# Kernel tuning notes

Hardware: AMD Instinct MI355X
Metric: run time of the kernel (lower is better)

Reference implementation:

```python
import jax, jax.numpy as jnp
import numpy as np

B, S, D = 4, 1024, 1024
NH, DH = 16, 64
DI = 4096
EPS = 1e-5


def layer_norm(x, g, b):
    mu = jnp.mean(x, axis=-1, keepdims=True)
    var = jnp.mean(jnp.square(x - mu), axis=-1, keepdims=True)
    return (x - mu) * jax.lax.rsqrt(var + EPS) * g + b


def rel_shift(x):
    # x: [B, n, q, r] -> Transformer-XL relative shift + lower-tri mask
    b, n, q, r = x.shape
    zp = jnp.zeros((b, n, q, 1), x.dtype)
    xp = jnp.concatenate([zp, x], axis=3).reshape(b, n, r + 1, q)
    x = xp[:, :, 1:, :].reshape(b, n, q, r)
    tril = jnp.tril(jnp.ones((q, r), x.dtype), r - q)
    return x * tril[None, None]


def setup_inputs() -> dict:
    key = jax.random.key(0)
    ks = jax.random.split(key, 16)
    sc = 0.02
    return {
        "w": jax.random.normal(ks[0], (B, S, D), jnp.float32),
        "r": jax.random.normal(ks[1], (B, S, D), jnp.float32),
        "w_bias": jax.random.normal(ks[2], (NH, 1, DH), jnp.float32) * sc,
        "r_bias": jax.random.normal(ks[3], (NH, 1, DH), jnp.float32) * sc,
        "Wq": jax.random.normal(ks[4], (D, NH * DH), jnp.float32) * sc,
        "Wk": jax.random.normal(ks[5], (D, NH * DH), jnp.float32) * sc,
        "Wv": jax.random.normal(ks[6], (D, NH * DH), jnp.float32) * sc,
        "Wr": jax.random.normal(ks[7], (D, NH * DH), jnp.float32) * sc,
        "Wo": jax.random.normal(ks[8], (NH * DH, D), jnp.float32) * sc,
        "ln1_g": jnp.ones((D,), jnp.float32),
        "ln1_b": jnp.zeros((D,), jnp.float32),
        "W1": jax.random.normal(ks[9], (D, DI), jnp.float32) * sc,
        "b1": jnp.zeros((DI,), jnp.float32),
        "W2": jax.random.normal(ks[10], (DI, D), jnp.float32) * sc,
        "b2": jnp.zeros((D,), jnp.float32),
        "ln2_g": jnp.ones((D,), jnp.float32),
        "ln2_b": jnp.zeros((D,), jnp.float32),
    }


def reference(w, r, w_bias, r_bias, Wq, Wk, Wv, Wr, Wo,
              ln1_g, ln1_b, W1, b1, W2, b2, ln2_g, ln2_b):
    b, q_len, _ = w.shape
    k_len = q_len
    scale = 1.0 / (DH ** 0.5)

    def heads(x):
        return x.reshape(b, -1, NH, DH).transpose(0, 2, 1, 3)  # [B, n, S, d]

    q = heads(w @ Wq)
    k = heads(w @ Wk)
    v = heads(w @ Wv)
    rr = heads(r @ Wr)

    ac = jnp.einsum('bnid,bnjd->bnij', q + w_bias[None], k)
    bd = rel_shift(jnp.einsum('bnid,bnjd->bnij', q + r_bias[None], rr))
    attn_score = (ac + bd) * scale

    mask = jnp.triu(jnp.ones((q_len, k_len), bool), 1)
    attn_score = jnp.where(mask[None, None], jnp.float32(-1e9), attn_score)
    attn_prob = jax.nn.softmax(attn_score, axis=-1)

    attn_vec = jnp.einsum('bnij,bnjd->bnid', attn_prob, v)
    attn_vec = attn_vec.transpose(0, 2, 1, 3).reshape(b, q_len, NH * DH)
    attn_out = attn_vec @ Wo

    x = layer_norm(w + attn_out, ln1_g, ln1_b)
    ff = jax.nn.relu(x @ W1 + b1) @ W2 + b2
    return layer_norm(x + ff, ln2_g, ln2_b)
```

## Files before the change

### kernel.cpp

```cpp
#include <hip/hip_runtime.h>
#include <hip/hip_bf16.h>

using bf16 = __hip_bfloat16;
typedef __attribute__((ext_vector_type(8))) short bf16x8;
typedef __attribute__((ext_vector_type(4))) float f32x4;

static constexpr int TB  = 4;
static constexpr int TS  = 1024;
static constexpr int TD  = 1024;
static constexpr int TNH = 16;
static constexpr int TDH = 64;
static constexpr int TDI = 4096;

__device__ __forceinline__ void gll16(const bf16* g, bf16* l)
{
    __builtin_amdgcn_global_load_lds(
        (const __attribute__((address_space(1))) void*)g,
        (__attribute__((address_space(3))) void*)l, 16, 0, 0);
}

__global__ __launch_bounds__(256) void zero_out_k(float* __restrict__ out, long n)
{
    long i = (long)blockIdx.x * 256 + threadIdx.x;
    if (i < n) out[i] = 0.0f;
}

__global__ __launch_bounds__(256) void convert2_f2b(const float* __restrict__ a,
                                                    const float* __restrict__ b,
                                                    bf16* __restrict__ oa,
                                                    bf16* __restrict__ ob, long n)
{
    const float* src = blockIdx.y ? b : a;
    bf16* dst = blockIdx.y ? ob : oa;
    long i = ((long)blockIdx.x * 256 + threadIdx.x) * 8;
    if (i >= n) return;
    float4 f0 = *(const float4*)(src + i);
    float4 f1 = *(const float4*)(src + i + 4);
    bf16 t[8] = {__float2bfloat16(f0.x), __float2bfloat16(f0.y),
                 __float2bfloat16(f0.z), __float2bfloat16(f0.w),
                 __float2bfloat16(f1.x), __float2bfloat16(f1.y),
                 __float2bfloat16(f1.z), __float2bfloat16(f1.w)};
    *(bf16x8*)(dst + i) = *(bf16x8*)t;
}

__global__ __launch_bounds__(256) void transpose_f2b(const float* __restrict__ in,
                                                     bf16* __restrict__ out,
                                                     int R, int C)
{
    __shared__ float tile[32][33];
    int c0 = blockIdx.x * 32, r0 = blockIdx.y * 32;
    int tx = threadIdx.x & 31, ty = threadIdx.x >> 5;
#pragma unroll
    for (int dy = 0; dy < 32; dy += 8)
        tile[ty + dy][tx] = in[(long)(r0 + ty + dy) * C + (c0 + tx)];
    __syncthreads();
#pragma unroll
    for (int dy = 0; dy < 32; dy += 8)
        out[(long)(c0 + ty + dy) * R + (r0 + tx)] = __float2bfloat16(tile[tx][ty + dy]);
}

__global__ __launch_bounds__(256) void transpose5_f2b(const float* __restrict__ p0,
                                                      const float* __restrict__ p1,
                                                      const float* __restrict__ p2,
                                                      const float* __restrict__ p3,
                                                      const float* __restrict__ p4,
                                                      bf16* __restrict__ dstBase)
{
    __shared__ float tile[32][33];
    const int D = TD;
    int z = blockIdx.z;
    const float* in = (z == 0) ? p0 : (z == 1) ? p1 : (z == 2) ? p2 : (z == 3) ? p3 : p4;
    bf16* out = dstBase + (long)z * D * D;
    int c0 = blockIdx.x * 32, r0 = blockIdx.y * 32;
    int tx = threadIdx.x & 31, ty = threadIdx.x >> 5;
#pragma unroll
    for (int dy = 0; dy < 32; dy += 8)
        tile[ty + dy][tx] = in[(long)(r0 + ty + dy) * D + (c0 + tx)];
    __syncthreads();
#pragma unroll
    for (int dy = 0; dy < 32; dy += 8)
        out[(long)(c0 + ty + dy) * D + (r0 + tx)] = __float2bfloat16(tile[tx][ty + dy]);
}


__device__ __forceinline__ void stage_half(const bf16* __restrict__ X, long ldx,
                                           long rbase, long kcol,
                                           bf16* lds, int srow)
{
    gll16(X + (rbase + srow) * ldx + kcol, lds);
    gll16(X + (rbase + 128 + srow) * ldx + kcol, lds + 4096);
}

template<int MODE>
__global__ __launch_bounds__(512, 2) void gemm256_k(
    const bf16* __restrict__ A, long lda,
    const bf16* __restrict__ Bt, long ldb,
    bf16* __restrict__ O0, bf16* __restrict__ O1,
    bf16* __restrict__ O2, bf16* __restrict__ O3,
    const float* __restrict__ bias,
    int K, int GY, long ldc)
{
    __shared__ bf16 LDSbf[65536];

    const int NT = K >> 6;
    const int NI = NT >> 1;

    const int nwg = gridDim.x;
    const int orig = blockIdx.x;
    const int q = nwg >> 3, r = nwg & 7;
    const int xcd = orig & 7, idx = orig >> 3;
    const int wgid = (xcd < r ? xcd * (q + 1) : r * (q + 1) + (xcd - r) * q) + idx;

    int tx, ty;
    if (MODE == 1) {
        if (wgid < 192) { ty = wgid & 15; tx = wgid >> 4; }
        else { int w2 = wgid - 192; ty = 16 + (w2 & 15); tx = 12 + (w2 >> 4); }
    } else {
        ty = wgid % GY; tx = wgid / GY;
    }
    const long row0 = (long)ty * 256;
    const int col0 = tx * 256;

    const int tid = threadIdx.x;
    const int lane = tid & 63;
    const int wave = tid >> 6;
    const int wm2 = wave >> 2;
    const int wn4 = wave & 3;
    const int l15 = lane & 15;
    const int lq  = lane >> 4;

    const int slot = ((l15 & 1) << 2) | (lq ^ ((l15 >> 1) & 3));
    const int rdA = (wm2 * 64 + (l15 >> 1)) * 64 + slot * 8;
    const int rdB = 16384 + (wn4 * 32 + (l15 >> 1)) * 64 + slot * 8;

    const int srow  = wave * 16 + ((lane >> 3) << 1) + ((lane >> 2) & 1);
    const int scol8 = ((lane & 3) ^ ((lane >> 3) & 3)) * 8;

    f32x4 acc[8][4] = {};
    bf16x8 af[8], bb[4];

#define SA(t, db, kh) stage_half(A, lda, row0, (long)(t) * 64 + (kh) * 32 + scol8, \
                                 LDSbf + (db) * 32768 + (kh) * 8192 + wave * 512, srow)
#define SB(t, db, kh) stage_half(Bt, ldb, (long)col0, (long)(t) * 64 + (kh) * 32 + scol8, \
                                 LDSbf + (db) * 32768 + 16384 + (kh) * 8192 + wave * 512, srow)
#define RD_A(bp, kh) do {                                                              \
    _Pragma("unroll")                                                                  \
    for (int i_ = 0; i_ < 8; ++i_)                                                     \
        af[i_] = *(const bf16x8*)(LDSbf + (bp) * 32768 + (kh) * 8192 + rdA + i_ * 512);\
    } while (0)
#define RD_B(bp, kh, jh) do {                                                          \
    bb[(jh)*2]   = *(const bf16x8*)(LDSbf + (bp)*32768 + (kh)*8192 + rdB + ((jh)*2)*512);   \
    bb[(jh)*2+1] = *(const bf16x8*)(LDSbf + (bp)*32768 + (kh)*8192 + rdB + ((jh)*2+1)*512); \
    } while (0)
#define MM(jh) do {                                                                    \
    __builtin_amdgcn_s_setprio(1);                                                     \
    _Pragma("unroll")                                                                  \
    for (int i_ = 0; i_ < 8; ++i_) {                                                   \
        acc[i_][(jh)*2]   = __builtin_amdgcn_mfma_f32_16x16x32_bf16(af[i_], bb[(jh)*2],   acc[i_][(jh)*2],   0, 0, 0); \
        acc[i_][(jh)*2+1] = __builtin_amdgcn_mfma_f32_16x16x32_bf16(af[i_], bb[(jh)*2+1], acc[i_][(jh)*2+1], 0, 0, 0); \
    }                                                                                  \
    __builtin_amdgcn_s_setprio(0);                                                     \
    } while (0)
#define BAR       __builtin_amdgcn_s_barrier()
#define WLGKM0    do { asm volatile("s_waitcnt lgkmcnt(0)" ::: "memory");              \
                       __builtin_amdgcn_sched_barrier(0); } while (0)
#define WVM6      asm volatile("s_waitcnt vmcnt(6)" ::: "memory")

    SA(0, 0, 0); SB(0, 0, 0); SA(0, 0, 1); SB(0, 0, 1); SA(1, 1, 0);
    WVM6; BAR;

    for (int it = 0; it < NI; ++it) {
        const int T  = 2 * it;
        const int t1 = T + 1;
        const int t2 = (T + 2 < NT) ? T + 2 : NT - 1;
        const int t3 = (T + 3 < NT) ? T + 3 : NT - 1;

        RD_A(0, 0); RD_B(0, 0, 0); SB(t1, 1, 0);
        BAR; WLGKM0; MM(0); BAR;
        RD_B(0, 0, 1); SA(t1, 1, 1);
        BAR; WLGKM0; MM(1); WVM6; BAR;
        RD_A(0, 1); RD_B(0, 1, 0); SB(t1, 1, 1);
        BAR; WLGKM0; MM(0); BAR;
        RD_B(0, 1, 1); SA(t2, 0, 0);
        BAR; WLGKM0; MM(1); WVM6; BAR;
        RD_A(1, 0); RD_B(1, 0, 0); SB(t2, 0, 0);
        BAR; WLGKM0; MM(0); BAR;
        RD_B(1, 0, 1); SA(t2, 0, 1);
        BAR; WLGKM0; MM(1); WVM6; BAR;
        RD_A(1, 1); RD_B(1, 1, 0); SB(t2, 0, 1);
        BAR; WLGKM0; MM(0); BAR;
        RD_B(1, 1, 1); SA(t3, 1, 0);
        BAR; WLGKM0; MM(1); WVM6; BAR;
    }
    asm volatile("s_waitcnt vmcnt(0)" ::: "memory");

#undef SA
#undef SB
#undef RD_A
#undef RD_B
#undef MM
#undef BAR
#undef WLGKM0
#undef WVM6

    if (MODE == 1) {
        const int sel = tx >> 2;
        bf16* O = (sel == 0) ? O0 : (sel == 1) ? O1 : (sel == 2) ? O2 : O3;
        const int coladj = sel << 10;
        const long rowadj = (sel == 3) ? 4096 : 0;
#pragma unroll
        for (int i = 0; i < 8; ++i) {
            long mrow0 = row0 - rowadj + wm2 * 128 + i * 16 + lq * 4;
#pragma unroll
            for (int j = 0; j < 4; ++j) {
                int nc = col0 - coladj + wn4 * 64 + j * 16 + l15;
#pragma unroll
                for (int rg = 0; rg < 4; ++rg) {
                    float v = acc[i][j][rg];
                    if (sel == 0) v += bias[nc];
                    long mrow = mrow0 + rg;
                    long b_ = mrow >> 10;
                    int s  = (int)mrow & 1023;
                    int n_ = nc >> 6, d = nc & 63;
                    long pidx;
                    if (sel == 2) {
                        pidx = ((b_ * 16 + n_) << 16)
                             + ((d >> 4) * 128 + (s >> 3)) * 128 + (d & 15) * 8 + (s & 7);
                    } else {
                        pidx = ((b_ * 16 + n_) << 16)
                             + ((s >> 4) * 8 + (d >> 3)) * 128 + (s & 15) * 8 + (d & 7);
                    }
                    O[pidx] = __float2bfloat16(v);
                }
            }
        }
    } else {
#pragma unroll
        for (int i = 0; i < 8; ++i) {
            long rb = (row0 + wm2 * 128 + i * 16 + lq * 4) * ldc;
#pragma unroll
            for (int j = 0; j < 4; ++j) {
                int nc = col0 + wn4 * 64 + j * 16 + l15;
#pragma unroll
                for (int rg = 0; rg < 4; ++rg) {
                    float v = acc[i][j][rg] + bias[nc];
                    v = fmaxf(v, 0.0f);
                    O0[rb + (long)rg * ldc + nc] = __float2bfloat16(v);
                }
            }
        }
    }
}

template<int MODE>
__global__ __launch_bounds__(512, 2) void gemm128_k(
    const bf16* __restrict__ A, long lda,
    const bf16* __restrict__ Bt, long ldb,
    float* __restrict__ Zf,
    const float* __restrict__ residf, const bf16* __restrict__ residb,
    const float* __restrict__ bias,
    int K, int GY, long ldc)
{
    __shared__ bf16 LDSbf[32768];

    const int NT = K >> 6;
    const int NI = NT >> 1;

    const int nwg = gridDim.x;
    const int orig = blockIdx.x;
    const int q = nwg >> 3, r = nwg & 7;
    const int xcd = orig & 7, idx = orig >> 3;
    const int wgid = (xcd < r ? xcd * (q + 1) : r * (q + 1) + (xcd - r) * q) + idx;

    const int ty = wgid % GY, tx = wgid / GY;
    const long row0 = (long)ty * 128;
    const long col0 = (long)tx * 128;

    const int tid = threadIdx.x;
    const int lane = tid & 63;
    const int wave = tid >> 6;
    const int wm2 = wave >> 2;
    const int wn4 = wave & 3;
    const int l15 = lane & 15;
    const int lq  = lane >> 4;

    const int slot = ((l15 & 1) << 2) | (lq ^ ((l15 >> 1) & 3));
    const int rdA = (wm2 * 32 + (l15 >> 1)) * 64 + slot * 8;
    const int rdB = 8192 + (wn4 * 16 + (l15 >> 1)) * 64 + slot * 8;

    const int srow  = (tid >> 3) * 2 + ((tid >> 2) & 1);
    const int scol8 = ((tid & 3) ^ ((tid >> 3) & 3)) * 8;

    f32x4 acc[4][2] = {};
    bf16x8 af[4], bb[2];

#define SA(t, db, kh) gll16(A + (row0 + srow) * lda + (long)(t) * 64 + (kh) * 32 + scol8, \
                            LDSbf + (db) * 16384 + (kh) * 4096 + wave * 512)
#define SB(t, db, kh) gll16(Bt + (col0 + srow) * ldb + (long)(t) * 64 + (kh) * 32 + scol8, \
                            LDSbf + (db) * 16384 + 8192 + (kh) * 4096 + wave * 512)
#define RD(db, kh) do {                                                                \
    _Pragma("unroll")                                                                  \
    for (int i_ = 0; i_ < 4; ++i_)                                                     \
        af[i_] = *(const bf16x8*)(LDSbf + (db) * 16384 + (kh) * 4096 + rdA + i_ * 512);\
    _Pragma("unroll")                                                                  \
    for (int j_ = 0; j_ < 2; ++j_)                                                     \
        bb[j_] = *(const bf16x8*)(LDSbf + (db) * 16384 + (kh) * 4096 + rdB + j_ * 512);\
    } while (0)
#define MM8 do {                                                                       \
    __builtin_amdgcn_s_setprio(1);                                                     \
    _Pragma("unroll")                                                                  \
    for (int i_ = 0; i_ < 4; ++i_) {                                                   \
        acc[i_][0] = __builtin_amdgcn_mfma_f32_16x16x32_bf16(af[i_], bb[0], acc[i_][0], 0, 0, 0); \
        acc[i_][1] = __builtin_amdgcn_mfma_f32_16x16x32_bf16(af[i_], bb[1], acc[i_][1], 0, 0, 0); \
    }                                                                                  \
    __builtin_amdgcn_s_setprio(0);                                                     \
    } while (0)
#define BAR       __builtin_amdgcn_s_barrier()
#define WLGKM0    do { asm volatile("s_waitcnt lgkmcnt(0)" ::: "memory");              \
                       __builtin_amdgcn_sched_barrier(0); } while (0)
#define WVM4      asm volatile("s_waitcnt vmcnt(4)" ::: "memory")

    SA(0, 0, 0); SB(0, 0, 0); SA(0, 0, 1); SB(0, 0, 1); SA(1, 1, 0); SB(1, 1, 0);
    WVM4; BAR;

    for (int it = 0; it < NI; ++it) {
        const int T  = 2 * it;
        const int t1 = T + 1;
        const int t2 = (T + 2 < NT) ? T + 2 : NT - 1;
        const int t3 = (T + 3 < NT) ? T + 3 : NT - 1;

        RD(0, 0); SA(t1, 1, 1); SB(t1, 1, 1);
        BAR; WLGKM0; MM8; WVM4; BAR;
        RD(0, 1); SA(t2, 0, 0); SB(t2, 0, 0);
        BAR; WLGKM0; MM8; WVM4; BAR;
        RD(1, 0); SA(t2, 0, 1); SB(t2, 0, 1);
        BAR; WLGKM0; MM8; WVM4; BAR;
        RD(1, 1); SA(t3, 1, 0); SB(t3, 1, 0);
        BAR; WLGKM0; MM8; WVM4; BAR;
    }
    asm volatile("s_waitcnt vmcnt(0)" ::: "memory");

#undef SA
#undef SB
#undef RD
#undef MM8
#undef BAR
#undef WLGKM0
#undef WVM4

#pragma unroll
    for (int i = 0; i < 4; ++i) {
        long mrow0 = row0 + wm2 * 64 + i * 16 + lq * 4;
#pragma unroll
        for (int j = 0; j < 2; ++j) {
            int nc = (int)col0 + wn4 * 32 + j * 16 + l15;
#pragma unroll
            for (int rg = 0; rg < 4; ++rg) {
                long ridx = (mrow0 + rg) * ldc + nc;
                float v = acc[i][j][rg];
                if (MODE == 3) v += residf[ridx];
                else           v += bias[nc] + __bfloat162float(residb[ridx]);
                Zf[ridx] = v;
            }
        }
    }
}

__global__ __launch_bounds__(64, 4) void flash_attn(
    const bf16* __restrict__ Qpk, const bf16* __restrict__ Kpk,
    const bf16* __restrict__ RRpk, const bf16* __restrict__ Vpk,
    const float* __restrict__ wbias, const float* __restrict__ rbias,
    bf16* __restrict__ Oa)
{
    const int S = TS, D = TD;
    __shared__ bf16 scr[16 * 161];

    const int orig = blockIdx.x;
    const int xcd = orig & 7, idx = orig >> 3;
    const int bn = xcd * 8 + (idx & 7);
    const int rem = idx >> 3;
    const int r16 = 63 - rem;
    const int it = r16 >> 3;
    const int rowstart = r16 * 16;
    const int dwq = (r16 & 7) * 16;
    const int b = bn >> 4, n = bn & 15;

    const int lane = threadIdx.x;
    const int l15 = lane & 15, lq = lane >> 4;

    const bf16* Qb = Qpk  + (long)bn * 65536;
    const bf16* Kb = Kpk  + (long)bn * 65536;
    const bf16* Rb = RRpk + (long)bn * 65536;
    const bf16* Vb = Vpk  + (long)bn * 65536;

    bf16x8 afw[2], afr[2];
#pragma unroll
    for (int ks = 0; ks < 2; ++ks) {
        afw[ks] = *(const bf16x8*)(Qb + (r16 * 8 + ks * 4 + lq) * 128 + l15 * 8);
        bf16 tmp[8];
#pragma unroll
        for (int jj = 0; jj < 8; ++jj) {
            int di_ = n * 64 + ks * 32 + lq * 8 + jj;
            float f = __bfloat162float(((const bf16*)&afw[ks])[jj])
                      + rbias[di_] - wbias[di_];
            tmp[jj] = __float2bfloat16(f);
        }
        afr[ks] = *(bf16x8*)tmp;
    }

    float mst[4], lst[4];
    f32x4 Oacc[4] = {};
#pragma unroll
    for (int rg = 0; rg < 4; ++rg) { mst[rg] = -1e30f; lst[rg] = 0.0f; }

    const int cofs16 = 1008 - rowstart;

    for (int jt = 0; jt <= it; ++jt) {
        const int j0 = jt * 128;
        const int rbt = (j0 + cofs16) >> 4;

#pragma unroll
        for (int g = 0; g < 2; ++g) {
            const int NF = g ? 4 : 5;
            f32x4 bdl[5] = {};
#pragma unroll
            for (int ks = 0; ks < 2; ++ks) {
                bf16x8 bfr[5];
#pragma unroll
                for (int f = 0; f < 5; ++f) {
                    if (f < NF) {
                        int t = rbt + g * 5 + f;
                        if (t > 63) t = 63;
                        bfr[f] = *(const bf16x8*)(Rb + (t * 8 + ks * 4 + lq) * 128 + l15 * 8);
                    }
                }
#pragma unroll
                for (int f = 0; f < 5; ++f)
                    if (f < NF)
                        bdl[f] = __builtin_amdgcn_mfma_f32_16x16x32_bf16(
                            afr[ks], bfr[f], bdl[f], 0, 0, 0);
            }
#pragma unroll
            for (int f = 0; f < 5; ++f)
                if (f < NF)
#pragma unroll
                    for (int rg = 0; rg < 4; ++rg) {
                        int ldi = lq * 4 + rg;
                        scr[ldi * 161 + (g * 5 + f) * 16 + l15] =
                            __float2bfloat16(bdl[f][rg]);
                    }
        }

        f32x4 ac[8] = {};
#pragma unroll
        for (int ks = 0; ks < 2; ++ks) {
            bf16x8 bk[8];
#pragma unroll
            for (int f = 0; f < 8; ++f)
                bk[f] = *(const bf16x8*)(
                    Kb + (((j0 >> 4) + f) * 8 + ks * 4 + lq) * 128 + l15 * 8);
#pragma unroll
            for (int f = 0; f < 8; ++f)
                ac[f] = __builtin_amdgcn_mfma_f32_16x16x32_bf16(
                    afw[ks], bk[f], ac[f], 0, 0, 0);
        }

        const bool diag = (jt == it);
#pragma unroll
        for (int nf = 0; nf < 8; ++nf)
#pragma unroll
            for (int rg = 0; rg < 4; ++rg) {
                int ldi = lq * 4 + rg;
                int col = nf * 16 + l15;
                float bdv = __bfloat162float(scr[ldi * 161 + (col + 15 - ldi)]);
                float s = (ac[nf][rg] + bdv) * 0.125f;
                if (diag && (col > dwq + ldi)) s = -1e30f;
                ac[nf][rg] = s;
            }

        float alpha[4];
#pragma unroll
        for (int rg = 0; rg < 4; ++rg) {
            float v = -1e30f;
#pragma unroll
            for (int nf = 0; nf < 8; ++nf) v = fmaxf(v, ac[nf][rg]);
            for (int o = 8; o; o >>= 1) v = fmaxf(v, __shfl_xor(v, o));
            float mn = fmaxf(mst[rg], v);
            alpha[rg] = __expf(mst[rg] - mn);
            mst[rg] = mn;
        }
#pragma unroll
        for (int nf = 0; nf < 8; ++nf)
#pragma unroll
            for (int rg = 0; rg < 4; ++rg)
                ac[nf][rg] = __expf(ac[nf][rg] - mst[rg]);
#pragma unroll
        for (int rg = 0; rg < 4; ++rg) {
            float sv = 0.0f;
#pragma unroll
            for (int nf = 0; nf < 8; ++nf) sv += ac[nf][rg];
            for (int o = 8; o; o >>= 1) sv += __shfl_xor(sv, o);
            lst[rg] = lst[rg] * alpha[rg] + sv;
        }
#pragma unroll
        for (int nf = 0; nf < 4; ++nf)
#pragma unroll
            for (int rg = 0; rg < 4; ++rg)
                Oacc[nf][rg] *= alpha[rg];

#pragma unroll
        for (int nf = 0; nf < 8; ++nf)
#pragma unroll
            for (int rg = 0; rg < 4; ++rg) {
                int ldi = lq * 4 + rg;
                scr[ldi * 136 + nf * 16 + l15] = __float2bfloat16(ac[nf][rg]);
            }
#pragma unroll
        for (int ks2 = 0; ks2 < 4; ++ks2) {
            bf16x8 pa = *(const bf16x8*)(&scr[l15 * 136 + ks2 * 32 + lq * 8]);
            bf16x8 vb[4];
#pragma unroll
            for (int nf = 0; nf < 4; ++nf)
                vb[nf] = *(const bf16x8*)(
                    Vb + (nf * 128 + (j0 >> 3) + ks2 * 4 + lq) * 128 + l15 * 8);
#pragma unroll
            for (int nf = 0; nf < 4; ++nf)
                Oacc[nf] = __builtin_amdgcn_mfma_f32_16x16x32_bf16(
                    pa, vb[nf], Oacc[nf], 0, 0, 0);
        }
    }

#pragma unroll
    for (int rg = 0; rg < 4; ++rg) {
        float inv = 1.0f / lst[rg];
#pragma unroll
        for (int nf = 0; nf < 4; ++nf) {
            int row = rowstart + lq * 4 + rg;
            int col = nf * 16 + l15;
            Oa[((long)(b * S + row)) * D + n * 64 + col] =
                __float2bfloat16(Oacc[nf][rg] * inv);
        }
    }
}

__global__ __launch_bounds__(256) void ln_single(const float* __restrict__ Zf,
                                                 const float* __restrict__ g,
                                                 const float* __restrict__ beta,
                                                 float* __restrict__ Yf,
                                                 bf16* __restrict__ Yb)
{
    const int D = TD;
    long row = blockIdx.x;
    int tid = threadIdx.x;
    int wave = tid >> 6;

    float v[4], s = 0.0f;
#pragma unroll
    for (int it = 0; it < 4; ++it) {
        int c = tid + it * 256;
        float x = Zf[row * D + c];
        v[it] = x; s += x;
    }
    for (int off = 32; off; off >>= 1) s += __shfl_xor(s, off);
    __shared__ float sm[8];
    if ((tid & 63) == 0) sm[wave] = s;
    __syncthreads();
    float mean = (sm[0] + sm[1] + sm[2] + sm[3]) * (1.0f / D);

    float var = 0.0f;
#pragma unroll
    for (int it = 0; it < 4; ++it) { float d = v[it] - mean; var += d * d; }
    for (int off = 32; off; off >>= 1) var += __shfl_xor(var, off);
    if ((tid & 63) == 0) sm[4 + wave] = var;
    __syncthreads();
    var = (sm[4] + sm[5] + sm[6] + sm[7]) * (1.0f / D);
    float rinv = rsqrtf(var + 1e-5f);

#pragma unroll
    for (int it = 0; it < 4; ++it) {
        int c = tid + it * 256;
        float o = (v[it] - mean) * rinv * g[c] + beta[c];
        if (Yf) Yf[row * D + c] = o;
        if (Yb) Yb[row * D + c] = __float2bfloat16(o);
    }
}

extern "C" void kernel_launch(void* const* d_in, const int* in_sizes, int n_in,
                              void* d_out, int out_size, void* d_ws, size_t ws_size,
                              hipStream_t stream)
{
    const float* w      = (const float*)d_in[0];
    const float* r      = (const float*)d_in[1];
    const float* w_bias = (const float*)d_in[2];
    const float* r_bias = (const float*)d_in[3];
    const float* Wq     = (const float*)d_in[4];
    const float* Wk     = (const float*)d_in[5];
    const float* Wv     = (const float*)d_in[6];
    const float* Wr     = (const float*)d_in[7];
    const float* Wo     = (const float*)d_in[8];
    const float* ln1_g  = (const float*)d_in[9];
    const float* ln1_b  = (const float*)d_in[10];
    const float* W1     = (const float*)d_in[11];
    const float* b1     = (const float*)d_in[12];
    const float* W2     = (const float*)d_in[13];
    const float* b2     = (const float*)d_in[14];
    const float* ln2_g  = (const float*)d_in[15];
    const float* ln2_b  = (const float*)d_in[16];
    float* out = (float*)d_out;

    const int  B = TB, S = TS, D = TD, NH = TNH, DH = TDH, DI = TDI;
    const long MS = (long)B * S;
    const long ND = (long)MS * D;

    char* base = (char*)d_ws;
    size_t off = 0;
    auto alloc = [&](size_t bytes) -> void* {
        void* p = base + off;
        off += (bytes + 255) & ~(size_t)255;
        return p;
    };
    bf16* wqT  = (bf16*)alloc(2UL * D * D);
    bf16* wkT  = (bf16*)alloc(2UL * D * D);
    bf16* wvT  = (bf16*)alloc(2UL * D * D);
    bf16* wrT  = (bf16*)alloc(2UL * D * D);
    bf16* woT  = (bf16*)alloc(2UL * D * D);
    bf16* w1T  = (bf16*)alloc(2UL * D * DI);
    bf16* w2T  = (bf16*)alloc(2UL * DI * D);
    bf16* bufA = (bf16*)alloc(2UL * ND);
    bf16* bufB = (bf16*)alloc(2UL * ND);
    bf16* Qpk  = (bf16*)alloc(2UL * ND);
    bf16* Kpk  = (bf16*)alloc(2UL * ND);
    bf16* RRpk = (bf16*)alloc(2UL * ND);
    bf16* Vpk  = (bf16*)alloc(2UL * ND);
    bf16* R0   = (bf16*)alloc(2UL * MS * DI);
    size_t need = off;
    (void)in_sizes; (void)n_in; (void)out_size;

    if (ws_size < need) {
        zero_out_k<<<dim3((unsigned)((ND + 255) / 256)), 256, 0, stream>>>(out, ND);
        return;
    }

    bf16* w_bf = bufA;  bf16* attn_vec = bufA;
    bf16* r_bf = bufB;  bf16* x_bf     = bufB;
    bf16* h    = R0;
    float* Pf  = (float*)Qpk;

    convert2_f2b<<<dim3((unsigned)(ND / (8 * 256)), 2), 256, 0, stream>>>(
        w, r, w_bf, r_bf, ND);
    transpose5_f2b<<<dim3(D / 32, D / 32, 5), 256, 0, stream>>>(
        Wq, Wk, Wv, Wr, Wo, wqT);
    transpose_f2b<<<dim3(DI / 32, D / 32), 256, 0, stream>>>(W1, w1T, D, DI);
    transpose_f2b<<<dim3(D / 32, DI / 32), 256, 0, stream>>>(W2, w2T, DI, D);

    gemm256_k<1><<<dim3(256, 1), 512, 0, stream>>>(
        w_bf, D, wqT, D, Qpk, Kpk, Vpk, RRpk, w_bias, D, 16, D);

    flash_attn<<<dim3(4096), 64, 0, stream>>>(Qpk, Kpk, RRpk, Vpk, w_bias, r_bias,
                                              attn_vec);

    gemm128_k<3><<<dim3(256, 1), 512, 0, stream>>>(
        attn_vec, D, woT, D, Pf, w, nullptr, nullptr, D, 32, D);
    ln_single<<<dim3((unsigned)MS), 256, 0, stream>>>(Pf, ln1_g, ln1_b, nullptr, x_bf);

    gemm256_k<2><<<dim3(256, 1), 512, 0, stream>>>(
        x_bf, D, w1T, D, h, nullptr, nullptr, nullptr, b1, D, 16, DI);

    gemm128_k<4><<<dim3(256, 1), 512, 0, stream>>>(
        h, DI, w2T, DI, Pf, nullptr, x_bf, b2, DI, 32, D);
    ln_single<<<dim3((unsigned)MS), 256, 0, stream>>>(Pf, ln2_g, ln2_b, out, nullptr);
}
```

Baseline: 370.6 us.

## Swizzle GEMM tile order into groups, vectorize V stores, raise MFMA priority

Both GEMM kernels now map workgroup IDs onto small rectangular groups of output tiles (4x4 or 8x4 blocks) rather than column-major order. The goal is better L2/MALL reuse of A and B panels across concurrently running workgroups. The transposed V-projection epilogue now writes four bf16 values as one 8-byte store instead of four scalar stores. The attention kernel wraps its MFMA bursts in s_setprio so waves issuing matrix ops get scheduling priority over waves doing loads or softmax. Together these touch scheduling, epilogue efficiency and cache locality, and the grouped mapping assumes the grid dimensions fit the hardcoded group sizes.

Result: no change. 370.6 us (+0.0%).

```diff
diff --git a/kernel.cpp b/kernel.cpp
--- a/kernel.cpp
+++ b/kernel.cpp
@@ -3,6 +3,7 @@
 
 using bf16 = __hip_bfloat16;
 typedef __attribute__((ext_vector_type(8))) short bf16x8;
+typedef __attribute__((ext_vector_type(4))) short bf16x4;
 typedef __attribute__((ext_vector_type(4))) float f32x4;
 
 static constexpr int TB  = 4;
@@ -112,11 +113,16 @@
     const int wgid = (xcd < r ? xcd * (q + 1) : r * (q + 1) + (xcd - r) * q) + idx;
 
     int tx, ty;
-    if (MODE == 1) {
-        if (wgid < 192) { ty = wgid & 15; tx = wgid >> 4; }
-        else { int w2 = wgid - 192; ty = 16 + (w2 & 15); tx = 12 + (w2 >> 4); }
-    } else {
-        ty = wgid % GY; tx = wgid / GY;
+    {
+        const int l = wgid & 15;
+        const int st = wgid >> 4;
+        const int lty = l & 3, ltx = l >> 2;
+        if (MODE == 1) {
+            if (st < 12) { ty = (st & 3) * 4 + lty; tx = (st >> 2) * 4 + ltx; }
+            else { int s2 = st - 12; ty = 16 + s2 * 4 + lty; tx = 12 + ltx; }
+        } else {
+            ty = (st & 3) * 4 + lty; tx = (st >> 2) * 4 + ltx;
+        }
     }
     const long row0 = (long)ty * 256;
     const int col0 = tx * 256;
@@ -214,23 +220,32 @@
 #pragma unroll
             for (int j = 0; j < 4; ++j) {
                 int nc = col0 - coladj + wn4 * 64 + j * 16 + l15;
-#pragma unroll
-                for (int rg = 0; rg < 4; ++rg) {
-                    float v = acc[i][j][rg];
-                    if (sel == 0) v += bias[nc];
-                    long mrow = mrow0 + rg;
-                    long b_ = mrow >> 10;
-                    int s  = (int)mrow & 1023;
+                if (sel == 2) {
+                    long b_ = mrow0 >> 10;
+                    int s  = (int)mrow0 & 1023;
                     int n_ = nc >> 6, d = nc & 63;
-                    long pidx;
-                    if (sel == 2) {
-                        pidx = ((b_ * 16 + n_) << 16)
-                             + ((d >> 4) * 128 + (s >> 3)) * 128 + (d & 15) * 8 + (s & 7);
-                    } else {
-                        pidx = ((b_ * 16 + n_) << 16)
-                             + ((s >> 4) * 8 + (d >> 3)) * 128 + (s & 15) * 8 + (d & 7);
+                    long pidx = ((b_ * 16 + n_) << 16)
+                              + ((d >> 4) * 128 + (s >> 3)) * 128
+                              + (d & 15) * 8 + (s & 7);
+                    bf16 t4[4];
+#pragma unroll
+                    for (int rg = 0; rg < 4; ++rg)
+                        t4[rg] = __float2bfloat16(acc[i][j][rg]);
+                    *(bf16x4*)(O + pidx) = *(bf16x4*)t4;
+                } else {
+#pragma unroll
+                    for (int rg = 0; rg < 4; ++rg) {
+                        float v = acc[i][j][rg];
+                        if (sel == 0) v += bias[nc];
+                        long mrow = mrow0 + rg;
+                        long b_ = mrow >> 10;
+                        int s  = (int)mrow & 1023;
+                        int n_ = nc >> 6, d = nc & 63;
+                        long pidx = ((b_ * 16 + n_) << 16)
+                                  + ((s >> 4) * 8 + (d >> 3)) * 128
+                                  + (s & 15) * 8 + (d & 7);
+                        O[pidx] = __float2bfloat16(v);
                     }
-                    O[pidx] = __float2bfloat16(v);
                 }
             }
         }
@@ -272,7 +287,10 @@
     const int xcd = orig & 7, idx = orig >> 3;
     const int wgid = (xcd < r ? xcd * (q + 1) : r * (q + 1) + (xcd - r) * q) + idx;
 
-    const int ty = wgid % GY, tx = wgid / GY;
+    const int l = wgid & 31;
+    const int sup = wgid >> 5;
+    const int ty = (sup & 3) * 8 + (l & 7);
+    const int tx = (sup >> 2) * 4 + (l >> 3);
     const long row0 = (long)ty * 128;
     const long col0 = (long)tx * 128;
 
@@ -434,11 +452,13 @@
                         bfr[f] = *(const bf16x8*)(Rb + (t * 8 + ks * 4 + lq) * 128 + l15 * 8);
                     }
                 }
+                __builtin_amdgcn_s_setprio(1);
 #pragma unroll
                 for (int f = 0; f < 5; ++f)
                     if (f < NF)
                         bdl[f] = __builtin_amdgcn_mfma_f32_16x16x32_bf16(
                             afr[ks], bfr[f], bdl[f], 0, 0, 0);
+                __builtin_amdgcn_s_setprio(0);
             }
 #pragma unroll
             for (int f = 0; f < 5; ++f)
@@ -459,10 +479,12 @@
             for (int f = 0; f < 8; ++f)
                 bk[f] = *(const bf16x8*)(
                     Kb + (((j0 >> 4) + f) * 8 + ks * 4 + lq) * 128 + l15 * 8);
+            __builtin_amdgcn_s_setprio(1);
 #pragma unroll
             for (int f = 0; f < 8; ++f)
                 ac[f] = __builtin_amdgcn_mfma_f32_16x16x32_bf16(
                     afw[ks], bk[f], ac[f], 0, 0, 0);
+            __builtin_amdgcn_s_setprio(0);
         }
 
         const bool diag = (jt == it);
@@ -523,10 +545,12 @@
             for (int nf = 0; nf < 4; ++nf)
                 vb[nf] = *(const bf16x8*)(
                     Vb + (nf * 128 + (j0 >> 3) + ks2 * 4 + lq) * 128 + l15 * 8);
+            __builtin_amdgcn_s_setprio(1);
 #pragma unroll
             for (int nf = 0; nf < 4; ++nf)
                 Oacc[nf] = __builtin_amdgcn_mfma_f32_16x16x32_bf16(
                     pa, vb[nf], Oacc[nf], 0, 0, 0);
+            __builtin_amdgcn_s_setprio(0);
         }
     }
 
```
